# Kernel tuning notes

Hardware: AMD Instinct MI355X
Metric: run time of the kernel (lower is better)

## Reference

```python
import jax, jax.numpy as jnp
import numpy as np

GRID_SIZE = 5
SPLINE_ORDER = 3
N_COEFF = GRID_SIZE + SPLINE_ORDER  # 8 basis functions per input feature
D_MODEL = 1024
D_FF = 4096


def make_grid(in_features):
    # uniform grid on [-1, 1] extended by spline_order knots each side
    h = 2.0 / GRID_SIZE
    g = np.arange(-SPLINE_ORDER, GRID_SIZE + SPLINE_ORDER + 1, dtype=np.float32) * h - 1.0
    return jnp.asarray(np.tile(g[None, :], (in_features, 1)))  # (in, G + 2k + 1)


def b_splines(x, grid):
    # x: (N, in) -> (N, in, G + k) via Cox-de Boor recursion
    xe = x[..., None]
    bases = ((xe >= grid[:, :-1]) & (xe < grid[:, 1:])).astype(x.dtype)
    for j in range(1, SPLINE_ORDER + 1):
        left = (xe - grid[:, : -(j + 1)]) / (grid[:, j:-1] - grid[:, : -(j + 1)])
        right = (grid[:, j + 1 :] - xe) / (grid[:, j + 1 :] - grid[:, 1:-j])
        bases = left * bases[..., :-1] + right * bases[..., 1:]
    return bases


def kan_linear(x, base_w, spline_w, grid):
    # x: (N, in); base_w: (out, in); spline_w: (out, in, C)
    base = jax.nn.silu(x) @ base_w.T
    b = b_splines(x, grid)                      # (N, in, C)
    spl = jnp.einsum('nic,oic->no', b, spline_w)
    return base + spl


def setup_inputs() -> dict:
    key = jax.random.key(0)
    ks = jax.random.split(key, 7)
    s_in = 1.0 / np.sqrt(D_MODEL)
    s_ff = 1.0 / np.sqrt(D_FF)
    return {
        'x': jax.random.normal(ks[0], (2, 2048, D_MODEL), jnp.float32),
        'base_w1': jax.random.normal(ks[1], (D_FF, D_MODEL), jnp.float32) * s_in,
        'spline_w1': jax.random.normal(ks[2], (D_FF, D_MODEL, N_COEFF), jnp.float32) * s_in * 0.1,
        'base_w2': jax.random.normal(ks[3], (D_FF, D_MODEL), jnp.float32) * s_in,
        'spline_w2': jax.random.normal(ks[4], (D_FF, D_MODEL, N_COEFF), jnp.float32) * s_in * 0.1,
        'base_w3': jax.random.normal(ks[5], (D_MODEL, D_FF), jnp.float32) * s_ff,
        'spline_w3': jax.random.normal(ks[6], (D_MODEL, D_FF, N_COEFF), jnp.float32) * s_ff * 0.1,
        'grid_in': make_grid(D_MODEL),
        'grid_ff': make_grid(D_FF),
    }


def reference(x, base_w1, spline_w1, base_w2, spline_w2, base_w3, spline_w3, grid_in, grid_ff):
    shp = x.shape
    x2 = x.reshape(-1, shp[-1])                      # (N, d_model)
    h = kan_linear(x2, base_w1, spline_w1, grid_in) * kan_linear(x2, base_w2, spline_w2, grid_in)
    out = kan_linear(h, base_w3, spline_w3, grid_ff)
    return out.reshape(shp)
```

## Files before the change

kernel.cpp:

```cpp
#include <hip/hip_runtime.h>
#include <hip/hip_bf16.h>
#include <cstdint>
#include <cstddef>
#include <type_traits>


#define D_MODEL 1024
#define D_FF    4096
#define NTOK    4096
#define NC      9
#define K1      (D_MODEL * NC)
#define K3      (D_FF * NC)
#define SPLITK2 16
#define CHUNK   1024

typedef __attribute__((ext_vector_type(8))) short bf16x8;
typedef __attribute__((ext_vector_type(4))) float f32x4;

__device__ __forceinline__ void kan_feat(float x, __hip_bfloat16* dst) {
  float s = x / (1.0f + __expf(-x));
  float B[11];
#pragma unroll
  for (int j = 0; j < 11; ++j) {
    float gj = -2.2f + 0.4f * j;
    B[j] = (x >= gj && x < gj + 0.4f) ? 1.0f : 0.0f;
  }
#pragma unroll
  for (int p = 1; p <= 3; ++p) {
    float inv = 1.0f / (0.4f * p);
#pragma unroll
    for (int i = 0; i + p < 11; ++i) {
      float gi = -2.2f + 0.4f * i;
      B[i] = (x - gi) * inv * B[i] + ((gi + 0.4f + 0.4f * p) - x) * inv * B[i + 1];
    }
  }
  dst[0] = __float2bfloat16(s);
#pragma unroll
  for (int c = 0; c < 8; ++c) dst[1 + c] = __float2bfloat16(B[c]);
}

__global__ void pack_kan_w(const float* __restrict__ bw, const float* __restrict__ sw,
                           __hip_bfloat16* __restrict__ W, int K, int inShift,
                           size_t oBase, size_t total) {
  size_t t = (size_t)blockIdx.x * blockDim.x + threadIdx.x;
  if (t >= total) return;
  size_t o = t >> inShift;
  size_t i = t & (((size_t)1 << inShift) - 1);
  float b = bw[t];
  const float4* sp = (const float4*)(sw + t * 8);
  float4 s0 = sp[0], s1 = sp[1];
  __hip_bfloat16* dst = W + (oBase + o) * (size_t)K + i * NC;
  dst[0] = __float2bfloat16(b);
  dst[1] = __float2bfloat16(s0.x);
  dst[2] = __float2bfloat16(s0.y);
  dst[3] = __float2bfloat16(s0.z);
  dst[4] = __float2bfloat16(s0.w);
  dst[5] = __float2bfloat16(s1.x);
  dst[6] = __float2bfloat16(s1.y);
  dst[7] = __float2bfloat16(s1.z);
  dst[8] = __float2bfloat16(s1.w);
}

__global__ void build_a1(const float* __restrict__ x, __hip_bfloat16* __restrict__ A1) {
  size_t t = (size_t)blockIdx.x * blockDim.x + threadIdx.x;
  if (t >= (size_t)NTOK * D_MODEL) return;
  size_t n = t >> 10;
  size_t i = t & 1023;
  kan_feat(x[t], A1 + n * (size_t)K1 + i * NC);
}

template <typename HT>
__global__ void glu_a3(const HT* __restrict__ Hc, __hip_bfloat16* __restrict__ A3c) {
  size_t t = (size_t)blockIdx.x * blockDim.x + threadIdx.x;
  if (t >= (size_t)CHUNK * D_FF) return;
  size_t n = t >> 12;
  size_t j = t & 4095;
  float h1, h2;
  if constexpr (std::is_same<HT, float>::value) {
    h1 = Hc[n * 8192 + j];
    h2 = Hc[n * 8192 + 4096 + j];
  } else {
    h1 = __bfloat162float(Hc[n * 8192 + j]);
    h2 = __bfloat162float(Hc[n * 8192 + 4096 + j]);
  }
  kan_feat(h1 * h2, A3c + n * (size_t)K3 + j * NC);
}

#define STAGE(Ts)                                                                        \
  {                                                                                      \
    const int _sl = ((Ts) & 3) * 32768;                                                  \
    const size_t _ko = (size_t)(Ts) * 64;                                                \
    __builtin_amdgcn_global_load_lds(                                                    \
        (const __attribute__((address_space(1))) void*)(gA0 + _ko),                      \
        (__attribute__((address_space(3))) void*)(lds_raw + _sl + dA0), 16, 0, 0);       \
    __builtin_amdgcn_global_load_lds(                                                    \
        (const __attribute__((address_space(1))) void*)(gA1 + _ko),                      \
        (__attribute__((address_space(3))) void*)(lds_raw + _sl + dA1), 16, 0, 0);       \
    __builtin_amdgcn_global_load_lds(                                                    \
        (const __attribute__((address_space(1))) void*)(gB0 + _ko),                      \
        (__attribute__((address_space(3))) void*)(lds_raw + _sl + dB0), 16, 0, 0);       \
    __builtin_amdgcn_global_load_lds(                                                    \
        (const __attribute__((address_space(1))) void*)(gB1 + _ko),                      \
        (__attribute__((address_space(3))) void*)(lds_raw + _sl + dB1), 16, 0, 0);       \
  }

template <typename CT>
__global__ __launch_bounds__(512, 2) void gemm256(
    const __hip_bfloat16* __restrict__ A, const __hip_bfloat16* __restrict__ Bw,
    CT* __restrict__ Cp, int N, int K, int kLen) {
  __shared__ __align__(16) char lds_raw[4 * 32768];

  const int tid = threadIdx.x;
  const int wid = tid >> 6, lane = tid & 63;
  const int wr = wid >> 2, wc = wid & 3;

  const int nwg = gridDim.x * gridDim.y;
  const int orig = blockIdx.y * gridDim.x + blockIdx.x;
  const int q = nwg >> 3, r = nwg & 7;
  const int xcd = orig & 7, lid = orig >> 3;
  const int wg = (xcd < r ? xcd * (q + 1) : r * (q + 1) + (xcd - r) * q) + lid;
  const int bx = wg % gridDim.x, by = wg / gridDim.x;

  const size_t brow = (size_t)by * 256;
  const size_t bcol = (size_t)bx * 256;
  const int kStart = (int)blockIdx.z * kLen;
  const int NT = kLen / 32;

  const int kbx = (lane & 3) ^ ((lane >> 3) & 3);
  const int rsub = lane >> 2;
  const char* gA0 = (const char*)A +
      ((brow + (size_t)(wid * 16 + rsub)) * (size_t)K + kStart + kbx * 8) * 2;
  const char* gA1 = (const char*)A +
      ((brow + 128 + (size_t)(wid * 16 + rsub)) * (size_t)K + kStart + kbx * 8) * 2;
  const char* gB0 = (const char*)Bw +
      ((bcol + (size_t)(wid * 16 + rsub)) * (size_t)K + kStart + kbx * 8) * 2;
  const char* gB1 = (const char*)Bw +
      ((bcol + 128 + (size_t)(wid * 16 + rsub)) * (size_t)K + kStart + kbx * 8) * 2;
  const int dA0 = wid * 1024;
  const int dA1 = 8192 + wid * 1024;
  const int dB0 = 16384 + wid * 1024;
  const int dB1 = 24576 + wid * 1024;

  const int fkb = (lane >> 4) ^ ((lane >> 1) & 3);
  const int aoff = (wr * 128 + (lane & 15)) * 64 + fkb * 16;
  const int boff = 16384 + (wc * 64 + (lane & 15)) * 64 + fkb * 16;

  f32x4 acc[8][4] = {};

  STAGE(0);
  STAGE(1);
  STAGE(2);
  asm volatile("s_waitcnt vmcnt(8)" ::: "memory");
  __builtin_amdgcn_s_barrier();

  for (int T = 0; T < NT; ++T) {
    if (T + 3 < NT) STAGE(T + 3);

    const int sl = (T & 3) * 32768;
    bf16x8 af[8], bfr[4];
#pragma unroll
    for (int mf = 0; mf < 8; ++mf)
      af[mf] = *(const bf16x8*)(lds_raw + sl + aoff + mf * 1024);
#pragma unroll
    for (int nf = 0; nf < 4; ++nf)
      bfr[nf] = *(const bf16x8*)(lds_raw + sl + boff + nf * 1024);

    __builtin_amdgcn_s_setprio(1);
#pragma unroll
    for (int mf = 0; mf < 8; ++mf)
#pragma unroll
      for (int nf = 0; nf < 4; ++nf)
        acc[mf][nf] =
            __builtin_amdgcn_mfma_f32_16x16x32_bf16(af[mf], bfr[nf], acc[mf][nf], 0, 0, 0);
    __builtin_amdgcn_s_setprio(0);

    if (T + 4 <= NT) {
      asm volatile("s_waitcnt vmcnt(8)" ::: "memory");
    } else if (T + 3 == NT) {
      asm volatile("s_waitcnt vmcnt(4)" ::: "memory");
    } else if (T + 2 == NT) {
      asm volatile("s_waitcnt vmcnt(0)" ::: "memory");
    }
    if (T + 1 < NT) {
      asm volatile("s_waitcnt lgkmcnt(0)" ::: "memory");
      __builtin_amdgcn_s_barrier();
    }
  }

#pragma unroll
  for (int mf = 0; mf < 8; ++mf)
#pragma unroll
    for (int nf = 0; nf < 4; ++nf) {
      const size_t r0 = brow + wr * 128 + mf * 16 + (lane >> 4) * 4;
      const size_t c0 = bcol + wc * 64 + nf * 16 + (lane & 15);
      const size_t M = (size_t)gridDim.y * 256;
      CT* C = Cp + (size_t)blockIdx.z * M * (size_t)N;
#pragma unroll
      for (int rr = 0; rr < 4; ++rr) {
        float v = acc[mf][nf][rr];
        if constexpr (std::is_same<CT, float>::value)
          C[(r0 + rr) * (size_t)N + c0] = v;
        else
          C[(r0 + rr) * (size_t)N + c0] = __float2bfloat16(v);
      }
    }
}

__global__ void reduceK(const float* __restrict__ P, float* __restrict__ out, size_t quarter) {
  size_t t = (size_t)blockIdx.x * blockDim.x + threadIdx.x;
  if (t >= quarter) return;
  const float4* p = (const float4*)P;
  float4 a = p[t];
#pragma unroll
  for (int s = 1; s < SPLITK2; ++s) {
    float4 b = p[(size_t)s * quarter + t];
    a.x += b.x; a.y += b.y; a.z += b.z; a.w += b.w;
  }
  ((float4*)out)[t] = a;
}

extern "C" void kernel_launch(void* const* d_in, const int* in_sizes, int n_in,
                              void* d_out, int out_size, void* d_ws, size_t ws_size,
                              hipStream_t stream) {
  const float* x   = (const float*)d_in[0];
  const float* bw1 = (const float*)d_in[1];
  const float* sw1 = (const float*)d_in[2];
  const float* bw2 = (const float*)d_in[3];
  const float* sw2 = (const float*)d_in[4];
  const float* bw3 = (const float*)d_in[5];
  const float* sw3 = (const float*)d_in[6];
  float* out = (float*)d_out;
  char* ws = (char*)d_ws;

  const size_t W12_B  = (size_t)8192 * K1 * 2;
  const size_t A1_B   = (size_t)NTOK * K1 * 2;
  const size_t A3C_B  = (size_t)CHUNK * K3 * 2;
  const size_t HF32_B = (size_t)NTOK * 8192 * 4;

  const bool hF32 = ws_size >= W12_B + A1_B + HF32_B;

  __hip_bfloat16* W12 = (__hip_bfloat16*)(ws);
  __hip_bfloat16* A1  = (__hip_bfloat16*)(ws + W12_B);
  __hip_bfloat16* W3  = A1;
  void*           Hv  = (void*)(ws + W12_B + A1_B);
  __hip_bfloat16* A3c = (__hip_bfloat16*)(ws);
  float*          Par = (float*)(ws + A3C_B);

  {
    size_t total = (size_t)D_FF * D_MODEL;
    int blocks = (int)((total + 255) / 256);
    pack_kan_w<<<blocks, 256, 0, stream>>>(bw1, sw1, W12, K1, 10, 0, total);
    pack_kan_w<<<blocks, 256, 0, stream>>>(bw2, sw2, W12, K1, 10, 4096, total);
  }
  {
    size_t total = (size_t)NTOK * D_MODEL;
    build_a1<<<(int)((total + 255) / 256), 256, 0, stream>>>(x, A1);
  }
  if (hF32)
    gemm256<float><<<dim3(8192 / 256, NTOK / 256, 1), 512, 0, stream>>>(
        A1, W12, (float*)Hv, 8192, K1, K1);
  else
    gemm256<__hip_bfloat16><<<dim3(8192 / 256, NTOK / 256, 1), 512, 0, stream>>>(
        A1, W12, (__hip_bfloat16*)Hv, 8192, K1, K1);
  {
    size_t total = (size_t)D_MODEL * D_FF;
    pack_kan_w<<<(int)((total + 255) / 256), 256, 0, stream>>>(bw3, sw3, W3, K3, 12, 0, total);
  }
  for (int c = 0; c < NTOK / CHUNK; ++c) {
    {
      size_t total = (size_t)CHUNK * D_FF;
      int blocks = (int)((total + 255) / 256);
      if (hF32)
        glu_a3<float><<<blocks, 256, 0, stream>>>(
            (const float*)Hv + (size_t)c * CHUNK * 8192, A3c);
      else
        glu_a3<__hip_bfloat16><<<blocks, 256, 0, stream>>>(
            (const __hip_bfloat16*)Hv + (size_t)c * CHUNK * 8192, A3c);
    }
    gemm256<float><<<dim3(D_MODEL / 256, CHUNK / 256, SPLITK2), 512, 0, stream>>>(
        A3c, W3, Par, D_MODEL, K3, K3 / SPLITK2);
    {
      size_t quarter = (size_t)CHUNK * D_MODEL / 4;
      reduceK<<<(int)((quarter + 255) / 256), 256, 0, stream>>>(
          Par, out + (size_t)c * CHUNK * D_MODEL, quarter);
    }
  }
}
```

Measured before the change: 1.188 ms.

## Split GEMM K-step into two phases and pair-pack feature/weight stores

The GEMM main loop is split into two half-steps: it loads half of the A fragments, issues the A prefetch, runs 16 MFMAs, then loads the other half and issues the B prefetch before the next 16 MFMAs. Extra barriers and sched_barriers interleave global-to-LDS traffic with compute and lower register pressure from held fragments. Separately, the pack, build_a1 and glu_a3 kernels now handle two elements per thread and write packed 32-bit words instead of individual bf16 stores. The cost is more barriers per K-step, which may stall waves if the phases are unbalanced.

```diff
diff --git a/kernel.cpp b/kernel.cpp
--- a/kernel.cpp
+++ b/kernel.cpp
@@ -17,7 +17,12 @@
 typedef __attribute__((ext_vector_type(8))) short bf16x8;
 typedef __attribute__((ext_vector_type(4))) float f32x4;
 
-__device__ __forceinline__ void kan_feat(float x, __hip_bfloat16* dst) {
+__device__ __forceinline__ unsigned short bf16b(float f) {
+  __hip_bfloat16 h = __float2bfloat16(f);
+  return __builtin_bit_cast(unsigned short, h);
+}
+
+__device__ __forceinline__ void kan_feat_u(float x, unsigned short* dst) {
   float s = x / (1.0f + __expf(-x));
   float B[11];
 #pragma unroll
@@ -34,59 +39,74 @@
       B[i] = (x - gi) * inv * B[i] + ((gi + 0.4f + 0.4f * p) - x) * inv * B[i + 1];
     }
   }
-  dst[0] = __float2bfloat16(s);
-#pragma unroll
-  for (int c = 0; c < 8; ++c) dst[1 + c] = __float2bfloat16(B[c]);
+  dst[0] = bf16b(s);
+#pragma unroll
+  for (int c = 0; c < 8; ++c) dst[1 + c] = bf16b(B[c]);
 }
 
 __global__ void pack_kan_w(const float* __restrict__ bw, const float* __restrict__ sw,
                            __hip_bfloat16* __restrict__ W, int K, int inShift,
-                           size_t oBase, size_t total) {
+                           size_t oBase, size_t totalPairs) {
   size_t t = (size_t)blockIdx.x * blockDim.x + threadIdx.x;
-  if (t >= total) return;
-  size_t o = t >> inShift;
-  size_t i = t & (((size_t)1 << inShift) - 1);
-  float b = bw[t];
-  const float4* sp = (const float4*)(sw + t * 8);
-  float4 s0 = sp[0], s1 = sp[1];
-  __hip_bfloat16* dst = W + (oBase + o) * (size_t)K + i * NC;
-  dst[0] = __float2bfloat16(b);
-  dst[1] = __float2bfloat16(s0.x);
-  dst[2] = __float2bfloat16(s0.y);
-  dst[3] = __float2bfloat16(s0.z);
-  dst[4] = __float2bfloat16(s0.w);
-  dst[5] = __float2bfloat16(s1.x);
-  dst[6] = __float2bfloat16(s1.y);
-  dst[7] = __float2bfloat16(s1.z);
-  dst[8] = __float2bfloat16(s1.w);
+  if (t >= totalPairs) return;
+  size_t o = t >> (inShift - 1);
+  size_t ip = (t & (((size_t)1 << (inShift - 1)) - 1)) * 2;
+  size_t e0 = (o << inShift) + ip;
+  float2 b = *(const float2*)(bw + e0);
+  const float4* sp = (const float4*)(sw + e0 * 8);
+  float4 s0 = sp[0], s1 = sp[1], s2 = sp[2], s3 = sp[3];
+  unsigned short h[18];
+  h[0] = bf16b(b.x);
+  h[1] = bf16b(s0.x); h[2] = bf16b(s0.y); h[3] = bf16b(s0.z); h[4] = bf16b(s0.w);
+  h[5] = bf16b(s1.x); h[6] = bf16b(s1.y); h[7] = bf16b(s1.z); h[8] = bf16b(s1.w);
+  h[9] = bf16b(b.y);
+  h[10] = bf16b(s2.x); h[11] = bf16b(s2.y); h[12] = bf16b(s2.z); h[13] = bf16b(s2.w);
+  h[14] = bf16b(s3.x); h[15] = bf16b(s3.y); h[16] = bf16b(s3.z); h[17] = bf16b(s3.w);
+  uint32_t* dst = (uint32_t*)(W + (oBase + o) * (size_t)K + ip * NC);
+#pragma unroll
+  for (int k = 0; k < 9; ++k) dst[k] = (uint32_t)h[2 * k] | ((uint32_t)h[2 * k + 1] << 16);
 }
 
 __global__ void build_a1(const float* __restrict__ x, __hip_bfloat16* __restrict__ A1) {
   size_t t = (size_t)blockIdx.x * blockDim.x + threadIdx.x;
-  if (t >= (size_t)NTOK * D_MODEL) return;
-  size_t n = t >> 10;
-  size_t i = t & 1023;
-  kan_feat(x[t], A1 + n * (size_t)K1 + i * NC);
+  if (t >= (size_t)NTOK * D_MODEL / 2) return;
+  size_t n = t >> 9;
+  size_t ip = (t & 511) * 2;
+  float2 xv = *(const float2*)(x + n * D_MODEL + ip);
+  unsigned short h[18];
+  kan_feat_u(xv.x, h);
+  kan_feat_u(xv.y, h + 9);
+  uint32_t* dst = (uint32_t*)(A1 + n * (size_t)K1 + ip * NC);
+#pragma unroll
+  for (int k = 0; k < 9; ++k) dst[k] = (uint32_t)h[2 * k] | ((uint32_t)h[2 * k + 1] << 16);
 }
 
 template <typename HT>
 __global__ void glu_a3(const HT* __restrict__ Hc, __hip_bfloat16* __restrict__ A3c) {
   size_t t = (size_t)blockIdx.x * blockDim.x + threadIdx.x;
-  if (t >= (size_t)CHUNK * D_FF) return;
-  size_t n = t >> 12;
-  size_t j = t & 4095;
-  float h1, h2;
+  if (t >= (size_t)CHUNK * D_FF / 2) return;
+  size_t n = t >> 11;
+  size_t jp = (t & 2047) * 2;
+  float a0, a1, c0, c1;
   if constexpr (std::is_same<HT, float>::value) {
-    h1 = Hc[n * 8192 + j];
-    h2 = Hc[n * 8192 + 4096 + j];
+    float2 u = *(const float2*)(Hc + n * 8192 + jp);
+    float2 v = *(const float2*)(Hc + n * 8192 + 4096 + jp);
+    a0 = u.x; a1 = u.y; c0 = v.x; c1 = v.y;
   } else {
-    h1 = __bfloat162float(Hc[n * 8192 + j]);
-    h2 = __bfloat162float(Hc[n * 8192 + 4096 + j]);
-  }
-  kan_feat(h1 * h2, A3c + n * (size_t)K3 + j * NC);
-}
-
-#define STAGE(Ts)                                                                        \
+    a0 = __bfloat162float(Hc[n * 8192 + jp]);
+    a1 = __bfloat162float(Hc[n * 8192 + jp + 1]);
+    c0 = __bfloat162float(Hc[n * 8192 + 4096 + jp]);
+    c1 = __bfloat162float(Hc[n * 8192 + 4096 + jp + 1]);
+  }
+  unsigned short h[18];
+  kan_feat_u(a0 * c0, h);
+  kan_feat_u(a1 * c1, h + 9);
+  uint32_t* dst = (uint32_t*)(A3c + n * (size_t)K3 + jp * NC);
+#pragma unroll
+  for (int k = 0; k < 9; ++k) dst[k] = (uint32_t)h[2 * k] | ((uint32_t)h[2 * k + 1] << 16);
+}
+
+#define STAGE_A(Ts)                                                                      \
   {                                                                                      \
     const int _sl = ((Ts) & 3) * 32768;                                                  \
     const size_t _ko = (size_t)(Ts) * 64;                                                \
@@ -96,6 +116,11 @@
     __builtin_amdgcn_global_load_lds(                                                    \
         (const __attribute__((address_space(1))) void*)(gA1 + _ko),                      \
         (__attribute__((address_space(3))) void*)(lds_raw + _sl + dA1), 16, 0, 0);       \
+  }
+#define STAGE_B(Ts)                                                                      \
+  {                                                                                      \
+    const int _sl = ((Ts) & 3) * 32768;                                                  \
+    const size_t _ko = (size_t)(Ts) * 64;                                                \
     __builtin_amdgcn_global_load_lds(                                                    \
         (const __attribute__((address_space(1))) void*)(gB0 + _ko),                      \
         (__attribute__((address_space(3))) void*)(lds_raw + _sl + dB0), 16, 0, 0);       \
@@ -147,31 +172,51 @@
 
   f32x4 acc[8][4] = {};
 
-  STAGE(0);
-  STAGE(1);
-  STAGE(2);
+  STAGE_A(0); STAGE_B(0);
+  STAGE_A(1); STAGE_B(1);
+  STAGE_A(2); STAGE_B(2);
   asm volatile("s_waitcnt vmcnt(8)" ::: "memory");
   __builtin_amdgcn_s_barrier();
 
   for (int T = 0; T < NT; ++T) {
-    if (T + 3 < NT) STAGE(T + 3);
-
     const int sl = (T & 3) * 32768;
-    bf16x8 af[8], bfr[4];
-#pragma unroll
-    for (int mf = 0; mf < 8; ++mf)
-      af[mf] = *(const bf16x8*)(lds_raw + sl + aoff + mf * 1024);
+
+    bf16x8 af0[4], bfr[4];
+#pragma unroll
+    for (int mf = 0; mf < 4; ++mf)
+      af0[mf] = *(const bf16x8*)(lds_raw + sl + aoff + mf * 1024);
 #pragma unroll
     for (int nf = 0; nf < 4; ++nf)
       bfr[nf] = *(const bf16x8*)(lds_raw + sl + boff + nf * 1024);
-
+    if (T + 3 < NT) STAGE_A(T + 3);
+    __builtin_amdgcn_s_barrier();
+    asm volatile("s_waitcnt lgkmcnt(0)" ::: "memory");
+    __builtin_amdgcn_sched_barrier(0);
     __builtin_amdgcn_s_setprio(1);
 #pragma unroll
-    for (int mf = 0; mf < 8; ++mf)
+    for (int mf = 0; mf < 4; ++mf)
 #pragma unroll
       for (int nf = 0; nf < 4; ++nf)
         acc[mf][nf] =
-            __builtin_amdgcn_mfma_f32_16x16x32_bf16(af[mf], bfr[nf], acc[mf][nf], 0, 0, 0);
+            __builtin_amdgcn_mfma_f32_16x16x32_bf16(af0[mf], bfr[nf], acc[mf][nf], 0, 0, 0);
+    __builtin_amdgcn_s_setprio(0);
+    __builtin_amdgcn_s_barrier();
+
+    bf16x8 af1[4];
+#pragma unroll
+    for (int mf = 0; mf < 4; ++mf)
+      af1[mf] = *(const bf16x8*)(lds_raw + sl + aoff + (mf + 4) * 1024);
+    if (T + 3 < NT) STAGE_B(T + 3);
+    __builtin_amdgcn_s_barrier();
+    asm volatile("s_waitcnt lgkmcnt(0)" ::: "memory");
+    __builtin_amdgcn_sched_barrier(0);
+    __builtin_amdgcn_s_setprio(1);
+#pragma unroll
+    for (int mf = 0; mf < 4; ++mf)
+#pragma unroll
+      for (int nf = 0; nf < 4; ++nf)
+        acc[mf + 4][nf] =
+            __builtin_amdgcn_mfma_f32_16x16x32_bf16(af1[mf], bfr[nf], acc[mf + 4][nf], 0, 0, 0);
     __builtin_amdgcn_s_setprio(0);
 
     if (T + 4 <= NT) {
@@ -181,10 +226,7 @@
     } else if (T + 2 == NT) {
       asm volatile("s_waitcnt vmcnt(0)" ::: "memory");
     }
-    if (T + 1 < NT) {
-      asm volatile("s_waitcnt lgkmcnt(0)" ::: "memory");
-      __builtin_amdgcn_s_barrier();
-    }
+    __builtin_amdgcn_s_barrier();
   }
 
 #pragma unroll
@@ -247,14 +289,14 @@
   float*          Par = (float*)(ws + A3C_B);
 
   {
-    size_t total = (size_t)D_FF * D_MODEL;
-    int blocks = (int)((total + 255) / 256);
-    pack_kan_w<<<blocks, 256, 0, stream>>>(bw1, sw1, W12, K1, 10, 0, total);
-    pack_kan_w<<<blocks, 256, 0, stream>>>(bw2, sw2, W12, K1, 10, 4096, total);
+    size_t pairs = (size_t)D_FF * D_MODEL / 2;
+    int blocks = (int)((pairs + 255) / 256);
+    pack_kan_w<<<blocks, 256, 0, stream>>>(bw1, sw1, W12, K1, 10, 0, pairs);
+    pack_kan_w<<<blocks, 256, 0, stream>>>(bw2, sw2, W12, K1, 10, 4096, pairs);
   }
   {
-    size_t total = (size_t)NTOK * D_MODEL;
-    build_a1<<<(int)((total + 255) / 256), 256, 0, stream>>>(x, A1);
+    size_t pairs = (size_t)NTOK * D_MODEL / 2;
+    build_a1<<<(int)((pairs + 255) / 256), 256, 0, stream>>>(x, A1);
   }
   if (hF32)
     gemm256<float><<<dim3(8192 / 256, NTOK / 256, 1), 512, 0, stream>>>(
@@ -263,13 +305,13 @@
     gemm256<__hip_bfloat16><<<dim3(8192 / 256, NTOK / 256, 1), 512, 0, stream>>>(
         A1, W12, (__hip_bfloat16*)Hv, 8192, K1, K1);
   {
-    size_t total = (size_t)D_MODEL * D_FF;
-    pack_kan_w<<<(int)((total + 255) / 256), 256, 0, stream>>>(bw3, sw3, W3, K3, 12, 0, total);
+    size_t pairs = (size_t)D_MODEL * D_FF / 2;
+    pack_kan_w<<<(int)((pairs + 255) / 256), 256, 0, stream>>>(bw3, sw3, W3, K3, 12, 0, pairs);
   }
   for (int c = 0; c < NTOK / CHUNK; ++c) {
     {
-      size_t total = (size_t)CHUNK * D_FF;
-      int blocks = (int)((total + 255) / 256);
+      size_t pairs = (size_t)CHUNK * D_FF / 2;
+      int blocks = (int)((pairs + 255) / 256);
       if (hF32)
         glu_a3<float><<<blocks, 256, 0, stream>>>(
             (const float*)Hv + (size_t)c * CHUNK * 8192, A3c);
```

New measurement: 1.184 ms. Within noise of the previous version (-0.3%).
